# Optimization experiments

Hardware: AMD Instinct MI355X
Metric: run time of the kernel (lower is better)

Reference implementation:

```python
import jax, jax.numpy as jnp
import numpy as np

POOL = 7  # pool_size
NUM_ROIS = 512


def setup_inputs() -> dict:
    key = jax.random.key(0)
    k_img, k_xy, k_wh = jax.random.split(key, 3)
    img = jax.random.normal(k_img, (1, 1024, 1024, 128), dtype=jnp.float32)
    xy = jax.random.randint(k_xy, (1, NUM_ROIS, 2), 0, 768)          # x1, y1
    wh = jax.random.randint(k_wh, (1, NUM_ROIS, 2), 16, 256)         # w, h  (>=16, fits in-bounds)
    rois = jnp.concatenate([xy, wh], axis=-1).astype(jnp.float32)    # (1, num_rois, 4) as (x1,y1,w,h)
    return {"img": img, "rois": rois}


def _axis_coords(start, size, in_limit):
    """TF1 resize_images bilinear (align_corners=False): src = dst * size/POOL.
    Returns absolute lo/hi gather indices and fractional weights, all length POOL."""
    scale = size.astype(jnp.float32) / POOL
    src = jnp.arange(POOL, dtype=jnp.float32) * scale        # within-crop coords
    lo = jnp.floor(src).astype(jnp.int32)
    lo = jnp.clip(lo, 0, size - 1)
    hi = jnp.clip(lo + 1, 0, size - 1)
    frac = src - lo.astype(jnp.float32)
    lo_abs = jnp.clip(start + lo, 0, in_limit - 1)
    hi_abs = jnp.clip(start + hi, 0, in_limit - 1)
    return lo_abs, hi_abs, frac


def reference(img, rois):
    # img: (1, H, W, C); rois: (1, num_rois, 4) -> out: (1, num_rois, POOL, POOL, C)
    img0 = img[0]
    H, W, C = img0.shape
    roi_i = rois[0].astype(jnp.int32)  # matches K.cast(..., 'int32')

    def one_roi(roi):
        x1, y1, w, h = roi[0], roi[1], roi[2], roi[3]
        y_lo, y_hi, fy = _axis_coords(y1, h, H)   # (POOL,)
        x_lo, x_hi, fx = _axis_coords(x1, w, W)   # (POOL,)
        v00 = img0[y_lo[:, None], x_lo[None, :], :]  # (POOL, POOL, C)
        v01 = img0[y_lo[:, None], x_hi[None, :], :]
        v10 = img0[y_hi[:, None], x_lo[None, :], :]
        v11 = img0[y_hi[:, None], x_hi[None, :], :]
        fx_ = fx[None, :, None]
        fy_ = fy[:, None, None]
        top = v00 * (1.0 - fx_) + v01 * fx_
        bot = v10 * (1.0 - fx_) + v11 * fx_
        return top * (1.0 - fy_) + bot * fy_

    out = jax.vmap(one_roi)(roi_i)  # (num_rois, POOL, POOL, C)
    return out[None]               # (1, num_rois, POOL, POOL, C)
```

## Files before the change

kernel.cpp:

```cpp
#include <hip/hip_runtime.h>


#define POOL 7
#define NUM_ROIS 512
#define IMG_H 1024
#define IMG_W 1024
#define IMG_C 128

__global__ __launch_bounds__(256) void roi_pool_kernel(
    const float* __restrict__ img,
    const float* __restrict__ rois,
    float* __restrict__ out)
{
    const int total = NUM_ROIS * POOL * POOL * 32;
    int idx = blockIdx.x * blockDim.x + threadIdx.x;
    if (idx >= total) return;

    const int c4  = idx & 31;
    const int p   = idx >> 5;
    const int px  = p % POOL;
    const int t   = p / POOL;
    const int py  = t % POOL;
    const int roi = t / POOL;

    const float* r = rois + (size_t)roi * 4;
    const int x1 = (int)r[0];
    const int y1 = (int)r[1];
    const int w  = (int)r[2];
    const int h  = (int)r[3];

    const float scy = (float)h / 7.0f;
    const float sy  = (float)py * scy;
    int ylo = (int)floorf(sy);
    ylo = min(max(ylo, 0), h - 1);
    const int yhi = min(max(ylo + 1, 0), h - 1);
    const float fy = sy - (float)ylo;
    const int ylo_abs = min(max(y1 + ylo, 0), IMG_H - 1);
    const int yhi_abs = min(max(y1 + yhi, 0), IMG_H - 1);

    const float scx = (float)w / 7.0f;
    const float sx  = (float)px * scx;
    int xlo = (int)floorf(sx);
    xlo = min(max(xlo, 0), w - 1);
    const int xhi = min(max(xlo + 1, 0), w - 1);
    const float fx = sx - (float)xlo;
    const int xlo_abs = min(max(x1 + xlo, 0), IMG_W - 1);
    const int xhi_abs = min(max(x1 + xhi, 0), IMG_W - 1);

    const int coff = c4 * 4;
    const size_t b00 = ((size_t)ylo_abs * IMG_W + xlo_abs) * IMG_C + coff;
    const size_t b01 = ((size_t)ylo_abs * IMG_W + xhi_abs) * IMG_C + coff;
    const size_t b10 = ((size_t)yhi_abs * IMG_W + xlo_abs) * IMG_C + coff;
    const size_t b11 = ((size_t)yhi_abs * IMG_W + xhi_abs) * IMG_C + coff;

    const float4 v00 = *(const float4*)(img + b00);
    const float4 v01 = *(const float4*)(img + b01);
    const float4 v10 = *(const float4*)(img + b10);
    const float4 v11 = *(const float4*)(img + b11);

    const float gx = 1.0f - fx;
    const float gy = 1.0f - fy;

    float4 o;
    o.x = (v00.x * gx + v01.x * fx) * gy + (v10.x * gx + v11.x * fx) * fy;
    o.y = (v00.y * gx + v01.y * fx) * gy + (v10.y * gx + v11.y * fx) * fy;
    o.z = (v00.z * gx + v01.z * fx) * gy + (v10.z * gx + v11.z * fx) * fy;
    o.w = (v00.w * gx + v01.w * fx) * gy + (v10.w * gx + v11.w * fx) * fy;

    *(float4*)(out + (size_t)p * IMG_C + coff) = o;
}

extern "C" void kernel_launch(void* const* d_in, const int* in_sizes, int n_in,
                              void* d_out, int out_size, void* d_ws, size_t ws_size,
                              hipStream_t stream) {
    const float* img  = (const float*)d_in[0];
    const float* rois = (const float*)d_in[1];
    float* out = (float*)d_out;

    const int total = NUM_ROIS * POOL * POOL * 32;
    const int block = 256;
    const int grid  = (total + block - 1) / block;
    roi_pool_kernel<<<grid, block, 0, stream>>>(img, rois, out);
}
```

Before: 15.91 us.

## Assign one wavefront per output row and loop over pooled columns

Each 64-lane wavefront now handles one (roi, py) output row. Each lane covers two channels with float2 loads and loops over the seven px positions, so ROI and y-coordinate math is computed once per row instead of per output pixel. Floor and clamp operations are simplified on the assumption that coordinates are non-negative. The trade-off is fewer threads, each with more serial loads, and narrower float2 accesses in place of float4.

```diff
diff --git a/kernel.cpp b/kernel.cpp
--- a/kernel.cpp
+++ b/kernel.cpp
@@ -6,22 +6,29 @@
 #define IMG_H 1024
 #define IMG_W 1024
 #define IMG_C 128
+#define NROWS (NUM_ROIS * POOL)
+
+__device__ __forceinline__ float2 lerp2(float2 v00, float2 v01, float2 v10,
+                                        float2 v11, float fx, float fy) {
+    const float gx = 1.0f - fx;
+    const float gy = 1.0f - fy;
+    float2 o;
+    o.x = (v00.x * gx + v01.x * fx) * gy + (v10.x * gx + v11.x * fx) * fy;
+    o.y = (v00.y * gx + v01.y * fx) * gy + (v10.y * gx + v11.y * fx) * fy;
+    return o;
+}
 
 __global__ __launch_bounds__(256) void roi_pool_kernel(
     const float* __restrict__ img,
     const float* __restrict__ rois,
     float* __restrict__ out)
 {
-    const int total = NUM_ROIS * POOL * POOL * 32;
-    int idx = blockIdx.x * blockDim.x + threadIdx.x;
-    if (idx >= total) return;
+    const int gtid = blockIdx.x * blockDim.x + threadIdx.x;
+    const int wid  = gtid >> 6;
+    const int lane = gtid & 63;
 
-    const int c4  = idx & 31;
-    const int p   = idx >> 5;
-    const int px  = p % POOL;
-    const int t   = p / POOL;
-    const int py  = t % POOL;
-    const int roi = t / POOL;
+    const int py  = wid % POOL;
+    const int roi = wid / POOL;
 
     const float* r = rois + (size_t)roi * 4;
     const int x1 = (int)r[0];
@@ -31,43 +38,37 @@
 
     const float scy = (float)h / 7.0f;
     const float sy  = (float)py * scy;
-    int ylo = (int)floorf(sy);
-    ylo = min(max(ylo, 0), h - 1);
-    const int yhi = min(max(ylo + 1, 0), h - 1);
+    int ylo = (int)sy;
+    ylo = min(ylo, h - 1);
+    const int yhi = min(ylo + 1, h - 1);
     const float fy = sy - (float)ylo;
     const int ylo_abs = min(max(y1 + ylo, 0), IMG_H - 1);
     const int yhi_abs = min(max(y1 + yhi, 0), IMG_H - 1);
 
+    const int coff = lane * 2;
+    const float* rowlo = img + (size_t)ylo_abs * IMG_W * IMG_C + coff;
+    const float* rowhi = img + (size_t)yhi_abs * IMG_W * IMG_C + coff;
+    float* orow = out + (size_t)wid * POOL * IMG_C + coff;
+
     const float scx = (float)w / 7.0f;
-    const float sx  = (float)px * scx;
-    int xlo = (int)floorf(sx);
-    xlo = min(max(xlo, 0), w - 1);
-    const int xhi = min(max(xlo + 1, 0), w - 1);
-    const float fx = sx - (float)xlo;
-    const int xlo_abs = min(max(x1 + xlo, 0), IMG_W - 1);
-    const int xhi_abs = min(max(x1 + xhi, 0), IMG_W - 1);
 
-    const int coff = c4 * 4;
-    const size_t b00 = ((size_t)ylo_abs * IMG_W + xlo_abs) * IMG_C + coff;
-    const size_t b01 = ((size_t)ylo_abs * IMG_W + xhi_abs) * IMG_C + coff;
-    const size_t b10 = ((size_t)yhi_abs * IMG_W + xlo_abs) * IMG_C + coff;
-    const size_t b11 = ((size_t)yhi_abs * IMG_W + xhi_abs) * IMG_C + coff;
+    #pragma unroll
+    for (int px = 0; px < POOL; ++px) {
+        const float sx = (float)px * scx;
+        int xlo = (int)sx;
+        xlo = min(xlo, w - 1);
+        const int xhi = min(xlo + 1, w - 1);
+        const float fx = sx - (float)xlo;
+        const int xlo_abs = min(max(x1 + xlo, 0), IMG_W - 1);
+        const int xhi_abs = min(max(x1 + xhi, 0), IMG_W - 1);
 
-    const float4 v00 = *(const float4*)(img + b00);
-    const float4 v01 = *(const float4*)(img + b01);
-    const float4 v10 = *(const float4*)(img + b10);
-    const float4 v11 = *(const float4*)(img + b11);
+        const float2 v00 = *(const float2*)(rowlo + (size_t)xlo_abs * IMG_C);
+        const float2 v01 = *(const float2*)(rowlo + (size_t)xhi_abs * IMG_C);
+        const float2 v10 = *(const float2*)(rowhi + (size_t)xlo_abs * IMG_C);
+        const float2 v11 = *(const float2*)(rowhi + (size_t)xhi_abs * IMG_C);
 
-    const float gx = 1.0f - fx;
-    const float gy = 1.0f - fy;
-
-    float4 o;
-    o.x = (v00.x * gx + v01.x * fx) * gy + (v10.x * gx + v11.x * fx) * fy;
-    o.y = (v00.y * gx + v01.y * fx) * gy + (v10.y * gx + v11.y * fx) * fy;
-    o.z = (v00.z * gx + v01.z * fx) * gy + (v10.z * gx + v11.z * fx) * fy;
-    o.w = (v00.w * gx + v01.w * fx) * gy + (v10.w * gx + v11.w * fx) * fy;
-
-    *(float4*)(out + (size_t)p * IMG_C + coff) = o;
+        *(float2*)(orow + (size_t)px * IMG_C) = lerp2(v00, v01, v10, v11, fx, fy);
+    }
 }
 
 extern "C" void kernel_launch(void* const* d_in, const int* in_sizes, int n_in,
@@ -77,8 +78,8 @@
     const float* rois = (const float*)d_in[1];
     float* out = (float*)d_out;
 
-    const int total = NUM_ROIS * POOL * POOL * 32;
+    const int total = NROWS * 64;
     const int block = 256;
-    const int grid  = (total + block - 1) / block;
+    const int grid  = total / block;
     roi_pool_kernel<<<grid, block, 0, stream>>>(img, rois, out);
 }
```

After: 15.50 us. -2.6%, faster.
